# Optimization experiments

Hardware: AMD Instinct MI355X
Metric: run time of the kernel (lower is better)

## Reference

```python
import jax, jax.numpy as jnp
import numpy as np

B, L, H, V = 64, 2048, 256, 32000
BETA = 0.9
EPS_K = 1e-6   # delta-rule key-norm eps (matches torch 1e-06)
EPS_LN = 1e-5  # torch LayerNorm default eps


def setup_inputs() -> dict:
    key = jax.random.key(0)
    ks = jax.random.split(key, 8)
    s = lambda k, shape: (jax.random.normal(k, shape, jnp.float32) * 0.02)
    return {
        "seq": jax.random.randint(ks[0], (B, L), 0, V),
        "embed": s(ks[1], (V, H)),
        "W1": s(ks[2], (H, 2 * H)),
        "b1": jnp.zeros((2 * H,), jnp.float32),
        "W2": s(ks[3], (2 * H, H)),
        "b2": jnp.zeros((H,), jnp.float32),
        "gamma": jnp.ones((H,), jnp.float32),
        "beta_ln": jnp.zeros((H,), jnp.float32),
        "rp_W": s(ks[4], (H, H)),
        "rp_b": jnp.zeros((H,), jnp.float32),
        "out_W": s(ks[5], (H, V)),
        "out_b": jnp.zeros((V,), jnp.float32),
    }


def reference(seq, embed, W1, b1, W2, b2, gamma, beta_ln, rp_W, rp_b, out_W, out_b):
    # Encoder: embed -> FFN residual -> LayerNorm
    e = embed[seq]                                    # [B, L, H]
    ff = jnp.maximum(e @ W1 + b1, 0.0) @ W2 + b2      # [B, L, H]
    x = e + ff
    mu = jnp.mean(x, axis=-1, keepdims=True)
    var = jnp.mean((x - mu) ** 2, axis=-1, keepdims=True)
    h_all = (x - mu) / jnp.sqrt(var + EPS_LN) * gamma + beta_ln  # [B, L, H]

    # Momentum delta-rule fast-weight memory over first L-1 steps (k == v == h_t)
    ks_t = jnp.moveaxis(h_all[:, :-1, :], 1, 0)       # [L-1, B, H] time-major

    def step(M, k):
        vp = jnp.einsum('bij,bj->bi', M, k)            # predicted value
        d = k - vp / (jnp.sum(k * k, axis=-1, keepdims=True) + EPS_K)
        delta = d[:, :, None] * k[:, None, :]          # outer product [B, H, H]
        return BETA * M + (1.0 - BETA) * delta, None

    M0 = jnp.zeros((h_all.shape[0], H, H), h_all.dtype)
    M, _ = jax.lax.scan(step, M0, ks_t)

    # Readout with final token
    y = jnp.einsum('bij,bj->bi', M, h_all[:, -1, :])   # [B, H]
    return (y @ rp_W + rp_b) @ out_W + out_b           # [B, V]
```

## Files before the change

kernel.cpp:

```cpp
#include <hip/hip_runtime.h>


#define B_ 64
#define L_ 2048
#define H_ 256
#define V_ 32000

typedef unsigned short u16;
typedef __attribute__((ext_vector_type(8))) short bf16x8;
typedef __attribute__((ext_vector_type(16))) float f32x16;
typedef __attribute__((ext_vector_type(4))) float f32x4;

__device__ __forceinline__ float b2f(u16 u){ union{unsigned x; float f;} z; z.x = ((unsigned)u)<<16; return z.f; }
__device__ __forceinline__ u16 f2b(float f){ union{float f; unsigned x;} z; z.f = f; unsigned r = z.x + 0x7FFFu + ((z.x>>16)&1u); return (u16)(r>>16); }
__device__ __forceinline__ float san(float v){ return (v == v && v > -1e30f && v < 1e30f) ? v : 0.f; }

template<bool F32> __device__ __forceinline__ float ldw(const void* p, long i){
  if (F32) return ((const float*)p)[i];
  return b2f(((const u16*)p)[i]);
}
template<bool F32> __device__ __forceinline__ float4 ld4(const void* p, long i){
  if (F32) return *(const float4*)((const float*)p + i);
  ushort4 u = *(const ushort4*)((const u16*)p + i);
  return make_float4(b2f(u.x), b2f(u.y), b2f(u.z), b2f(u.w));
}

__device__ __forceinline__ int detect_f32(const void* embed){
  const u16* e = (const u16*)embed;
  unsigned v = e[2 * (threadIdx.x & 255)];
  int ex = (v >> 7) & 0xFF;
  int pl = (ex >= 0x66 && ex <= 0x7D) || ((v & 0x7FFFu) == 0u);
  int cnt = __syncthreads_count(pl);
  return cnt < 128;
}

__global__ __launch_bounds__(256) void sentinel_kernel(const void* embed, void* out, float val)
{
  int f32 = detect_f32(embed);
  long idx = (long)blockIdx.x * 256 + threadIdx.x;
  if (idx < (long)B_ * V_){
    if (f32) ((float*)out)[idx] = val;
    else     ((u16*)out)[idx]   = f2b(val);
  }
}

template<bool F32>
__device__ __forceinline__ void wprep_body(
    const void* __restrict__ W1, const void* __restrict__ W2,
    u16* __restrict__ w1f_hi, u16* __restrict__ w1f_lo,
    u16* __restrict__ w2f_hi, u16* __restrict__ w2f_lo)
{
  const int cid = blockIdx.x * 256 + threadIdx.x;
  const int lane = cid & 63;
  const int nl = lane & 31, kh = lane >> 5;
  if (cid < 16384){
    const int nt = cid >> 10, k16 = (cid >> 6) & 15;
    const int n = nt*32 + nl;
    const int k0 = k16*16 + kh*8;
    #pragma unroll
    for (int e = 0; e < 8; ++e){
      float v = ldw<F32>(W1, (long)(k0+e)*512 + n);
      unsigned bi = __float_as_uint(v);
      u16 hi = (u16)(bi >> 16);
      float hif = __uint_as_float(((unsigned)hi) << 16);
      w1f_hi[cid*8 + e] = hi;
      w1f_lo[cid*8 + e] = f2b(v - hif);
    }
  } else {
    const int c2 = cid - 16384;
    const int nt = c2 >> 11, k16 = (c2 >> 6) & 31;
    const int n = nt*32 + nl;
    const int k0 = k16*16 + kh*8;
    #pragma unroll
    for (int e = 0; e < 8; ++e){
      float v = ldw<F32>(W2, (long)(k0+e)*256 + n);
      unsigned bi = __float_as_uint(v);
      u16 hi = (u16)(bi >> 16);
      float hif = __uint_as_float(((unsigned)hi) << 16);
      w2f_hi[c2*8 + e] = hi;
      w2f_lo[c2*8 + e] = f2b(v - hif);
    }
  }
}

__global__ __launch_bounds__(256) void wprep_kernel(
    const void* __restrict__ embed,
    const void* __restrict__ W1, const void* __restrict__ W2,
    u16* __restrict__ wbuf)
{
  u16* w1h = wbuf;
  u16* w1l = wbuf + 131072;
  u16* w2h = wbuf + 262144;
  u16* w2l = wbuf + 393216;
  if (detect_f32(embed)) wprep_body<true >(W1, W2, w1h, w1l, w2h, w2l);
  else                   wprep_body<false>(W1, W2, w1h, w1l, w2h, w2l);
}

template<bool F32>
__device__ __forceinline__ void encm_body(
    u16* e_l, u16* t1_l, float* red, float* red2, float* stats,
    const int* __restrict__ seq, const void* __restrict__ embed,
    const u16* __restrict__ w1f_hi, const u16* __restrict__ w1f_lo,
    const u16* __restrict__ w2f_hi, const u16* __restrict__ w2f_lo,
    const void* __restrict__ b1, const void* __restrict__ b2,
    const void* __restrict__ gamma, const void* __restrict__ beta,
    u16* __restrict__ h)
{
  const int tid = threadIdx.x;
  const long tok0 = (long)blockIdx.x * 32;
  const int lane = tid & 63, wv = tid >> 6;
  const int col = lane & 31, hw = lane >> 5;

  {
    const int tr = tid >> 3, u0 = (tid & 7) * 4;
    int tk = seq[tok0 + tr];
    tk = (tk >= 0 && tk < V_) ? tk : 0;
    #pragma unroll
    for (int c = 0; c < 4; ++c){
      const int u = u0 + c;
      const int phys = u ^ (tr & 7);
      if (F32){
        const float4* sp = (const float4*)((const float*)embed + (long)tk*H_ + u*8);
        float4 v0 = sp[0], v1 = sp[1];
        ushort4 o0, o1;
        o0.x=f2b(v0.x); o0.y=f2b(v0.y); o0.z=f2b(v0.z); o0.w=f2b(v0.w);
        o1.x=f2b(v1.x); o1.y=f2b(v1.y); o1.z=f2b(v1.z); o1.w=f2b(v1.w);
        *(ushort4*)&e_l[tr*256 + phys*8]     = o0;
        *(ushort4*)&e_l[tr*256 + phys*8 + 4] = o1;
      } else {
        uint4 v = *(const uint4*)((const u16*)embed + (long)tk*H_ + u*8);
        *(uint4*)&e_l[tr*256 + phys*8] = v;
      }
    }
  }
  __syncthreads();

  {
    f32x16 acc[4];
    #pragma unroll
    for (int t = 0; t < 4; ++t)
      #pragma unroll
      for (int r = 0; r < 16; ++r) acc[t][r] = 0.f;

    #pragma unroll
    for (int k16 = 0; k16 < 16; ++k16){
      const int phys = (k16*2 + hw) ^ (col & 7);
      bf16x8 a = *(const bf16x8*)&e_l[col*256 + phys*8];
      #pragma unroll
      for (int t = 0; t < 4; ++t){
        const int off = (((wv*4 + t)*16 + k16)*64 + lane)*8;
        bf16x8 bh = *(const bf16x8*)&w1f_hi[off];
        bf16x8 bl = *(const bf16x8*)&w1f_lo[off];
        acc[t] = __builtin_amdgcn_mfma_f32_32x32x16_bf16(a, bh, acc[t], 0, 0, 0);
        acc[t] = __builtin_amdgcn_mfma_f32_32x32x16_bf16(a, bl, acc[t], 0, 0, 0);
      }
    }

    #pragma unroll
    for (int t = 0; t < 4; ++t){
      const int n = (wv*4 + t)*32 + col;
      const float bb = ldw<F32>(b1, n);
      const int u = n >> 3, nl = n & 7;
      #pragma unroll
      for (int r = 0; r < 16; ++r){
        const int m = (r&3) + 8*(r>>2) + 4*hw;
        float v = fmaxf(acc[t][r] + bb, 0.f);
        t1_l[m*512 + ((u ^ (m&7))<<3) + nl] = f2b(v);
      }
    }
  }
  __syncthreads();

  f32x16 acc2[2];
  #pragma unroll
  for (int t = 0; t < 2; ++t)
    #pragma unroll
    for (int r = 0; r < 16; ++r) acc2[t][r] = 0.f;

  #pragma unroll
  for (int k16 = 0; k16 < 32; ++k16){
    const int phys = (k16*2 + hw) ^ (col & 7);
    bf16x8 a = *(const bf16x8*)&t1_l[col*512 + phys*8];
    #pragma unroll
    for (int t = 0; t < 2; ++t){
      const int off = (((wv*2 + t)*32 + k16)*64 + lane)*8;
      bf16x8 bh = *(const bf16x8*)&w2f_hi[off];
      bf16x8 bl = *(const bf16x8*)&w2f_lo[off];
      acc2[t] = __builtin_amdgcn_mfma_f32_32x32x16_bf16(a, bh, acc2[t], 0, 0, 0);
      acc2[t] = __builtin_amdgcn_mfma_f32_32x32x16_bf16(a, bl, acc2[t], 0, 0, 0);
    }
  }
  __syncthreads();

  u16* xb = t1_l;
  #pragma unroll
  for (int t = 0; t < 2; ++t){
    const int n = (wv*2 + t)*32 + col;
    const float bb = ldw<F32>(b2, n);
    const int ue = n >> 3, nl = n & 7;
    #pragma unroll
    for (int r = 0; r < 16; ++r){
      const int m = (r&3) + 8*(r>>2) + 4*hw;
      float ev = b2f(e_l[m*256 + ((ue ^ (m&7))<<3) + nl]);
      float x = acc2[t][r] + bb + ev;
      xb[m*256 + n] = f2b(x);
    }
  }
  __syncthreads();

  {
    const int row = tid >> 3, seg = tid & 7;
    const u16* xr = &xb[row*256 + seg*32];
    float s = 0.f, q = 0.f;
    #pragma unroll
    for (int j = 0; j < 32; j += 4){
      ushort4 v4 = *(const ushort4*)&xr[j];
      float v0 = b2f(v4.x), v1 = b2f(v4.y), v2 = b2f(v4.z), v3 = b2f(v4.w);
      s += v0 + v1 + v2 + v3;
      q += v0*v0 + v1*v1 + v2*v2 + v3*v3;
    }
    red[row*8 + seg] = s;
    red2[row*8 + seg] = q;
  }
  __syncthreads();
  if (tid < 32){
    float s = 0.f, q = 0.f;
    #pragma unroll
    for (int j = 0; j < 8; ++j){ s += red[tid*8 + j]; q += red2[tid*8 + j]; }
    float mu = s * (1.f/256.f);
    float var = q * (1.f/256.f) - mu*mu;
    stats[tid] = mu;
    stats[32 + tid] = 1.f / sqrtf(fmaxf(var, 0.f) + 1e-5f);
  }
  __syncthreads();

  {
    const int row = tid >> 3, c0 = (tid & 7) * 32;
    const float mu = stats[row], rs = stats[32 + row];
    u16* hp = h + (tok0 + row)*H_ + c0;
    const u16* xr = &xb[row*256 + c0];
    #pragma unroll
    for (int j = 0; j < 32; j += 4){
      float4 g  = ld4<F32>(gamma, c0 + j);
      float4 be = ld4<F32>(beta,  c0 + j);
      ushort4 xv = *(const ushort4*)&xr[j];
      ushort4 o;
      o.x = f2b(san((b2f(xv.x) - mu)*rs*g.x + be.x));
      o.y = f2b(san((b2f(xv.y) - mu)*rs*g.y + be.y));
      o.z = f2b(san((b2f(xv.z) - mu)*rs*g.z + be.z));
      o.w = f2b(san((b2f(xv.w) - mu)*rs*g.w + be.w));
      *(ushort4*)&hp[j] = o;
    }
  }
}

__global__ __launch_bounds__(256) void encm_kernel(
    const int* __restrict__ seq, const void* __restrict__ embed,
    const u16* __restrict__ wbuf,
    const void* __restrict__ b1, const void* __restrict__ b2,
    const void* __restrict__ gamma, const void* __restrict__ beta,
    u16* __restrict__ h)
{
  __shared__ __align__(16) u16 e_l[32*256];
  __shared__ __align__(16) u16 t1_l[32*512];
  __shared__ float red[256];
  __shared__ float red2[256];
  __shared__ float stats[64];
  const u16* w1h = wbuf;
  const u16* w1l = wbuf + 131072;
  const u16* w2h = wbuf + 262144;
  const u16* w2l = wbuf + 393216;
  if (detect_f32(embed))
    encm_body<true >(e_l, t1_l, red, red2, stats, seq, embed, w1h, w1l, w2h, w2l, b1, b2, gamma, beta, h);
  else
    encm_body<false>(e_l, t1_l, red, red2, stats, seq, embed, w1h, w1l, w2h, w2l, b1, b2, gamma, beta, h);
}

template<bool F32>
__device__ __forceinline__ void enc_body(
    u16* sm,
    const int* __restrict__ seq, const void* __restrict__ embed,
    const void* __restrict__ W1, const void* __restrict__ b1,
    const void* __restrict__ W2, const void* __restrict__ b2,
    const void* __restrict__ gamma, const void* __restrict__ beta,
    u16* __restrict__ h)
{
  u16* eT  = sm;
  u16* t1T = sm + 8192;
  u16* xb  = sm + 24576;
  float* stats = (float*)sm;

  const int tid = threadIdx.x;
  const long tok0 = (long)blockIdx.x * 32;

  for (int idx = tid; idx < 8192; idx += 256){
    int r = idx >> 8, c = idx & 255;
    int tk = seq[tok0 + r];
    tk = (tk >= 0 && tk < V_) ? tk : 0;
    eT[c*32 + r] = f2b(ldw<F32>(embed, (long)tk*H_ + c));
  }
  __syncthreads();

  const int jg = tid & 31, rg = tid >> 5;
  const int r0 = rg * 4;

  for (int sl = 0; sl < 4; ++sl){
    const int j0 = sl*128 + jg*4;
    float acc[4][4] = {{0.f}};
    for (int c = 0; c < 256; ++c){
      ushort4 a4 = *(const ushort4*)&eT[c*32 + r0];
      float4 w = ld4<F32>(W1, (long)c*512 + j0);
      float a0=b2f(a4.x), a1=b2f(a4.y), a2=b2f(a4.z), a3=b2f(a4.w);
      acc[0][0]+=a0*w.x; acc[0][1]+=a0*w.y; acc[0][2]+=a0*w.z; acc[0][3]+=a0*w.w;
      acc[1][0]+=a1*w.x; acc[1][1]+=a1*w.y; acc[1][2]+=a1*w.z; acc[1][3]+=a1*w.w;
      acc[2][0]+=a2*w.x; acc[2][1]+=a2*w.y; acc[2][2]+=a2*w.z; acc[2][3]+=a2*w.w;
      acc[3][0]+=a3*w.x; acc[3][1]+=a3*w.y; acc[3][2]+=a3*w.z; acc[3][3]+=a3*w.w;
    }
    for (int jj = 0; jj < 4; ++jj){
      float bb = ldw<F32>(b1, j0+jj);
      ushort4 o;
      o.x = f2b(fmaxf(acc[0][jj]+bb, 0.f));
      o.y = f2b(fmaxf(acc[1][jj]+bb, 0.f));
      o.z = f2b(fmaxf(acc[2][jj]+bb, 0.f));
      o.w = f2b(fmaxf(acc[3][jj]+bb, 0.f));
      *(ushort4*)&t1T[(j0+jj)*32 + r0] = o;
    }
  }
  __syncthreads();

  for (int sl = 0; sl < 2; ++sl){
    const int co0 = sl*128 + jg*4;
    float acc[4][4] = {{0.f}};
    for (int c = 0; c < 512; ++c){
      ushort4 a4 = *(const ushort4*)&t1T[c*32 + r0];
      float4 w = ld4<F32>(W2, (long)c*256 + co0);
      float a0=b2f(a4.x), a1=b2f(a4.y), a2=b2f(a4.z), a3=b2f(a4.w);
      acc[0][0]+=a0*w.x; acc[0][1]+=a0*w.y; acc[0][2]+=a0*w.z; acc[0][3]+=a0*w.w;
      acc[1][0]+=a1*w.x; acc[1][1]+=a1*w.y; acc[1][2]+=a1*w.z; acc[1][3]+=a1*w.w;
      acc[2][0]+=a2*w.x; acc[2][1]+=a2*w.y; acc[2][2]+=a2*w.z; acc[2][3]+=a2*w.w;
      acc[3][0]+=a3*w.x; acc[3][1]+=a3*w.y; acc[3][2]+=a3*w.z; acc[3][3]+=a3*w.w;
    }
    float bb0 = ldw<F32>(b2, co0+0), bb1 = ldw<F32>(b2, co0+1);
    float bb2 = ldw<F32>(b2, co0+2), bb3 = ldw<F32>(b2, co0+3);
    for (int rr = 0; rr < 4; ++rr){
      float x0 = acc[rr][0] + bb0 + b2f(eT[(co0+0)*32 + r0+rr]);
      float x1 = acc[rr][1] + bb1 + b2f(eT[(co0+1)*32 + r0+rr]);
      float x2 = acc[rr][2] + bb2 + b2f(eT[(co0+2)*32 + r0+rr]);
      float x3 = acc[rr][3] + bb3 + b2f(eT[(co0+3)*32 + r0+rr]);
      ushort4 o; o.x=f2b(x0); o.y=f2b(x1); o.z=f2b(x2); o.w=f2b(x3);
      *(ushort4*)&xb[(r0+rr)*256 + co0] = o;
    }
  }
  __syncthreads();

  if (tid < 32){
    float s = 0.f, q = 0.f;
    for (int c = 0; c < 256; ++c){ float v = b2f(xb[tid*256 + c]); s += v; q += v*v; }
    float mu = s * (1.f/256.f);
    float var = q * (1.f/256.f) - mu*mu;
    stats[tid] = mu;
    stats[32 + tid] = 1.f / sqrtf(fmaxf(var, 0.f) + 1e-5f);
  }
  __syncthreads();
  for (int idx = tid; idx < 8192; idx += 256){
    int r = idx >> 8, c = idx & 255;
    float hv = (b2f(xb[idx]) - stats[r]) * stats[32+r] * ldw<F32>(gamma, c) + ldw<F32>(beta, c);
    h[(tok0 + r)*H_ + c] = f2b(san(hv));
  }
}

__global__ __launch_bounds__(256) void enc_kernel(
    const int* __restrict__ seq, const void* __restrict__ embed,
    const void* __restrict__ W1, const void* __restrict__ b1,
    const void* __restrict__ W2, const void* __restrict__ b2,
    const void* __restrict__ gamma, const void* __restrict__ beta,
    u16* __restrict__ h)
{
  __shared__ __align__(16) u16 sm[32768];
  if (detect_f32(embed)) enc_body<true >(sm, seq, embed, W1, b1, W2, b2, gamma, beta, h);
  else                   enc_body<false>(sm, seq, embed, W1, b1, W2, b2, gamma, beta, h);
}

__global__ __launch_bounds__(64) void winv_kernel(
    const u16* __restrict__ h, u16* __restrict__ w2g, float* __restrict__ scg)
{
  __shared__ __align__(16) u16 k_l[32*256];
  __shared__ float g_l[32*33];
  __shared__ float w_l[32*33];
  __shared__ float bp[33];

  const int tid = threadIdx.x;
  const int cb = blockIdx.x;
  const int b = cb >> 6, ch = cb & 63;
  const int col = tid & 31, hw = tid >> 5;
  const int C = (ch == 63) ? 31 : 32;

  if (tid < 33) bp[tid] = powf(0.9f, (float)tid);

  {
    const int t = tid >> 1, u0 = (tid & 1) * 16;
    const u16* src = h + ((long)b*L_ + ch*32 + t)*H_ + u0*8;
    #pragma unroll
    for (int c = 0; c < 16; ++c){
      uint4 v = make_uint4(0u,0u,0u,0u);
      if (t < C) v = *(const uint4*)(src + c*8);
      int phys = (u0 + c) ^ (t & 7);
      *(uint4*)&k_l[t*256 + phys*8] = v;
    }
  }
  __syncthreads();

  {
    f32x16 acc; for (int r = 0; r < 16; ++r) acc[r] = 0.f;
    #pragma unroll
    for (int s = 0; s < 16; ++s){
      int phys = (s*2 + hw) ^ (col & 7);
      bf16x8 a = *(const bf16x8*)&k_l[col*256 + phys*8];
      acc = __builtin_amdgcn_mfma_f32_32x32x16_bf16(a, a, acc, 0, 0, 0);
    }
    #pragma unroll
    for (int r = 0; r < 16; ++r){
      int row = (r&3) + 8*(r>>2) + 4*hw;
      g_l[row*33 + col] = acc[r];
    }
  }
  __syncthreads();

  if (tid < 32){
    const int c = tid;
    for (int t = 0; t < 32; ++t){
      float acc = (t == c) ? 1.f : 0.f;
      if (t > c){
        float f = 0.1f / (g_l[t*33 + t] + 1e-6f);
        for (int s = c; s < t; ++s)
          acc -= f * bp[t-1-s] * g_l[t*33 + s] * w_l[s*33 + c];
      }
      w_l[t*33 + c] = acc;
    }
    scg[(long)cb*32 + c] = bp[c] / (g_l[c*33 + c] + 1e-6f);
  }
  __syncthreads();

  for (int idx = tid; idx < 1024; idx += 64){
    int t = idx >> 5, s = idx & 31;
    float v = 0.f;
    if (t < C && s <= t) v = 0.1f * bp[C-1-t] * w_l[t*33 + s];
    w2g[(long)cb*1024 + idx] = f2b(v);
  }
}

__global__ __launch_bounds__(512, 4) void scan_big(
    const u16* __restrict__ h, const u16* __restrict__ w2g,
    const float* __restrict__ scg, float* __restrict__ y)
{
  __shared__ __align__(16) u16   k_l[2][32*256];
  __shared__ __align__(16) u16   M_hi[32*256];
  __shared__ __align__(16) u16   M_lo[32*256];
  __shared__ float u_p[32*33];
  __shared__ __align__(16) u16   w2_l[32*32];
  __shared__ __align__(16) u16   dwT[32*32];
  __shared__ float sc_l[32];

  const int tid = threadIdx.x;
  const int b = blockIdx.x & 63, ib = blockIdx.x >> 6;
  const int lane = tid & 63, wv = tid >> 6;
  const int col = lane & 31, hw = lane >> 5;

  const u16*  hb  = h   + (long)b * L_ * H_;
  const u16*  w2b = w2g + (long)b * 64 * 1024;
  const float* scb = scg + (long)b * 64 * 32;

  const float b31 = powf(0.9f, 31.0f);
  const float b32 = b31 * 0.9f;

  for (int idx = tid; idx < 1024; idx += 512){
    ((uint4*)M_hi)[idx] = make_uint4(0u,0u,0u,0u);
    ((uint4*)M_lo)[idx] = make_uint4(0u,0u,0u,0u);
  }
  if (tid < 256){
    const int st = tid >> 3, su0 = (tid & 7) * 4;
    const u16* src = hb + (long)st * H_ + su0 * 8;
    #pragma unroll
    for (int c = 0; c < 4; ++c){
      uint4 v = *(const uint4*)(src + c*8);
      *(uint4*)&k_l[0][st*256 + ((su0+c)^(st&7))*8] = v;
    }
    *(uint2*)&w2_l[tid*4] = *(const uint2*)(w2b + tid*4);
    if (tid < 32) sc_l[tid] = scb[tid];
  }
  __syncthreads();

  for (int ch = 0; ch < 64; ++ch){
    const int cur = ch & 1, nxt = cur ^ 1;
    const float bC = (ch == 63) ? b31 : b32;

    uint2 pw = make_uint2(0u,0u); float psc = 0.f;

    if (wv < 4){
      const int th = wv & 1, ih = wv >> 1;
      const int li = lane & 15, kg = lane >> 4;
      const int t = th*16 + li;
      const int i = ih*16 + li;
      const int tx = t & 7, ix = i & 7;
      const u16* kr  = &k_l[cur][t*256];
      const u16* mhr = &M_hi[i*256];
      const u16* mlr = &M_lo[i*256];
      f32x4 a0, a1;
      #pragma unroll
      for (int r = 0; r < 4; ++r){ a0[r] = 0.f; a1[r] = 0.f; }
      #pragma unroll
      for (int ks = 0; ks < 8; ++ks){
        const int u = ks*4 + kg;
        bf16x8 a  = *(const bf16x8*)&kr[(u ^ tx)*8];
        bf16x8 bh = *(const bf16x8*)&mhr[(u ^ ix)*8];
        bf16x8 bl = *(const bf16x8*)&mlr[(u ^ ix)*8];
        if (ks & 1){
          a1 = __builtin_amdgcn_mfma_f32_16x16x32_bf16(a, bh, a1, 0, 0, 0);
          a1 = __builtin_amdgcn_mfma_f32_16x16x32_bf16(a, bl, a1, 0, 0, 0);
        } else {
          a0 = __builtin_amdgcn_mfma_f32_16x16x32_bf16(a, bh, a0, 0, 0, 0);
          a0 = __builtin_amdgcn_mfma_f32_16x16x32_bf16(a, bl, a0, 0, 0, 0);
        }
      }
      #pragma unroll
      for (int r = 0; r < 4; ++r)
        u_p[(th*16 + kg*4 + r)*33 + i] = a0[r] + a1[r];
    } else {
      const int s = tid - 256;
      const int st = s >> 3, su0 = (s & 7) * 4;
      const int chn = (ch < 63) ? ch + 1 : 63;
      const long tg = (long)chn*32 + st;
      const u16* src = hb + tg * H_ + su0 * 8;
      uint4 pf[4];
      #pragma unroll
      for (int c = 0; c < 4; ++c) pf[c] = *(const uint4*)(src + c*8);
      if (tg >= 2047){
        #pragma unroll
        for (int c = 0; c < 4; ++c) pf[c] = make_uint4(0u,0u,0u,0u);
      }
      pw = *(const uint2*)(w2b + chn*1024 + s*4);
      psc = (s < 32) ? scb[chn*32 + s] : 0.f;
      #pragma unroll
      for (int c = 0; c < 4; ++c)
        *(uint4*)&k_l[nxt][st*256 + ((su0+c)^(st&7))*8] = pf[c];
    }
    __syncthreads();

    if (wv == 0){
      const int jg = ib*32 + col;
      const int ju = jg >> 3, jo = jg & 7;
      bf16x8 bh0, bl0, bh1, bl1;
      #pragma unroll
      for (int c = 0; c < 8; ++c){
        const int t = hw*8 + c;
        float u = u_p[t*33 + col];
        float kti = b2f(k_l[cur][t*256 + ((ju ^ (t&7))<<3) + jo]);
        float r = kti - sc_l[t]*u;
        unsigned bi = __float_as_uint(r);
        bh0[c] = (short)(bi >> 16);
        bl0[c] = (short)f2b(r - __uint_as_float(bi & 0xFFFF0000u));
        const int t2 = t + 16;
        float u2 = u_p[t2*33 + col];
        float kti2 = b2f(k_l[cur][t2*256 + ((ju ^ (t2&7))<<3) + jo]);
        float r2 = kti2 - sc_l[t2]*u2;
        unsigned bi2 = __float_as_uint(r2);
        bh1[c] = (short)(bi2 >> 16);
        bl1[c] = (short)f2b(r2 - __uint_as_float(bi2 & 0xFFFF0000u));
      }
      f32x16 d0, d1;
      #pragma unroll
      for (int r = 0; r < 16; ++r){ d0[r] = 0.f; d1[r] = 0.f; }
      {
        bf16x8 aw0 = *(const bf16x8*)&w2_l[col*32 + hw*8];
        bf16x8 aw1 = *(const bf16x8*)&w2_l[col*32 + 16 + hw*8];
        d0 = __builtin_amdgcn_mfma_f32_32x32x16_bf16(aw0, bh0, d0, 0, 0, 0);
        d0 = __builtin_amdgcn_mfma_f32_32x32x16_bf16(aw0, bl0, d0, 0, 0, 0);
        d1 = __builtin_amdgcn_mfma_f32_32x32x16_bf16(aw1, bh1, d1, 0, 0, 0);
        d1 = __builtin_amdgcn_mfma_f32_32x32x16_bf16(aw1, bl1, d1, 0, 0, 0);
      }
      #pragma unroll
      for (int g = 0; g < 4; ++g){
        ushort4 o;
        o.x = f2b(d0[4*g+0] + d1[4*g+0]);
        o.y = f2b(d0[4*g+1] + d1[4*g+1]);
        o.z = f2b(d0[4*g+2] + d1[4*g+2]);
        o.w = f2b(d0[4*g+3] + d1[4*g+3]);
        *(ushort4*)&dwT[col*32 + 8*g + 4*hw] = o;
      }
    }
    __syncthreads();

    {
      bf16x8 bD0 = *(const bf16x8*)&dwT[col*32 + hw*8];
      bf16x8 bD1 = *(const bf16x8*)&dwT[col*32 + 16 + hw*8];
      const int j = wv*32 + col;
      const int ju = j >> 3, jo = j & 7;
      bf16x8 aK0, aK1;
      #pragma unroll
      for (int c = 0; c < 8; ++c){
        const int t = hw*8 + c;
        aK0[c] = (short)k_l[cur][t*256 + ((ju ^ (t&7))<<3) + jo];
        const int t2 = t + 16;
        aK1[c] = (short)k_l[cur][t2*256 + ((ju ^ (t2&7))<<3) + jo];
      }
      f32x16 macc;
      #pragma unroll
      for (int r = 0; r < 16; ++r) macc[r] = 0.f;
      macc = __builtin_amdgcn_mfma_f32_32x32x16_bf16(aK0, bD0, macc, 0, 0, 0);
      macc = __builtin_amdgcn_mfma_f32_32x32x16_bf16(aK1, bD1, macc, 0, 0, 0);
      #pragma unroll
      for (int g = 0; g < 4; ++g){
        const int u = wv*4 + g;
        const int addr = col*256 + ((u ^ (col&7))<<3) + 4*hw;
        ushort4 mh = *(ushort4*)&M_hi[addr];
        ushort4 ml = *(ushort4*)&M_lo[addr];
        ushort4 nh, nl;
        #pragma unroll
        for (int e = 0; e < 4; ++e){
          float f = b2f((&mh.x)[e]) + b2f((&ml.x)[e]);
          float nv = bC*f + macc[4*g + e];
          unsigned bi = __float_as_uint(nv);
          u16 hi = (u16)(bi >> 16);
          (&nh.x)[e] = hi;
          (&nl.x)[e] = f2b(nv - __uint_as_float(((unsigned)hi) << 16));
        }
        *(ushort4*)&M_hi[addr] = nh;
        *(ushort4*)&M_lo[addr] = nl;
      }
    }
    if (wv >= 4){
      const int s = tid - 256;
      *(uint2*)&w2_l[s*4] = pw;
      if (s < 32) sc_l[s] = psc;
    }
    __syncthreads();
  }

  float* q_l = u_p;
  float* par = u_p + 256;
  if (tid < 256) q_l[tid] = b2f(hb[(long)(L_-1)*H_ + tid]);
  __syncthreads();
  {
    const int i = tid & 31, pt = tid >> 5;
    float s = 0.f;
    #pragma unroll
    for (int jj = 0; jj < 16; ++jj){
      const int j = pt*16 + jj;
      const int addr = i*256 + (((j>>3) ^ (i&7))<<3) + (j&7);
      s += (b2f(M_hi[addr]) + b2f(M_lo[addr])) * q_l[j];
    }
    par[pt*32 + i] = s;
  }
  __syncthreads();
  if (tid < 32){
    float s = 0.f;
    #pragma unroll
    for (int pt = 0; pt < 16; ++pt) s += par[pt*32 + tid];
    y[b*H_ + ib*32 + tid] = san(s);
  }
}

__global__ __launch_bounds__(128) void scan_fallback(
    const u16* __restrict__ h, float* __restrict__ y)
{
  __shared__ __align__(16) float M_l[32*257];
  __shared__ __align__(16) u16  k_l[32*256];
  __shared__ float d_l[32*33];
  __shared__ float g_l[32*33];
  __shared__ float bp[33];

  const int tid = threadIdx.x;
  const int b = blockIdx.x & 63, ib = blockIdx.x >> 6;
  const int lane = tid & 63, wv = tid >> 6;
  const int col = lane & 31, hw = lane >> 5;

  for (int idx = tid; idx < 32*257; idx += 128) M_l[idx] = 0.f;
  if (tid < 33) bp[tid] = powf(0.9f, (float)tid);
  const u16* hb = h + (long)b * L_ * H_;
  __syncthreads();

  for (int ch = 0; ch < 64; ++ch){
    const int t0 = ch*32;
    const int C = (2047 - t0 < 32) ? (2047 - t0) : 32;

    {
      const int t = tid >> 2, j0 = (tid & 3) * 64;
      const uint4* gp = (const uint4*)(hb + (long)(t0 + t)*H_ + j0);
      #pragma unroll
      for (int c = 0; c < 8; ++c){
        uint4 v = (t < C) ? gp[c] : make_uint4(0u,0u,0u,0u);
        int phys = ((j0 >> 3) + c) ^ (t & 7);
        *(uint4*)&k_l[t*256 + phys*8] = v;
      }
    }
    __syncthreads();

    if (wv == 1){
      f32x16 acc; for (int r=0;r<16;++r) acc[r]=0.f;
      #pragma unroll
      for (int s = 0; s < 16; ++s){
        int phys = (s*2 + hw) ^ (col & 7);
        bf16x8 a = *(const bf16x8*)&k_l[col*256 + phys*8];
        acc = __builtin_amdgcn_mfma_f32_32x32x16_bf16(a, a, acc, 0, 0, 0);
      }
      #pragma unroll
      for (int r = 0; r < 16; ++r){
        int row = (r&3) + 8*(r>>2) + 4*hw;
        g_l[row*33 + col] = acc[r];
      }
    } else {
      f32x16 acc; for (int r=0;r<16;++r) acc[r]=0.f;
      for (int s = 0; s < 16; ++s){
        int phys = (s*2 + hw) ^ (col & 7);
        bf16x8 a = *(const bf16x8*)&k_l[col*256 + phys*8];
        bf16x8 bh, bl;
        const float* mp = &M_l[col*257 + s*16 + hw*8];
        #pragma unroll
        for (int c = 0; c < 8; ++c){
          float f = mp[c];
          unsigned bi = __float_as_uint(f);
          bh[c] = (short)(bi >> 16);
          float hif = __uint_as_float(bi & 0xFFFF0000u);
          bl[c] = (short)f2b(f - hif);
        }
        acc = __builtin_amdgcn_mfma_f32_32x32x16_bf16(a, bh, acc, 0, 0, 0);
        acc = __builtin_amdgcn_mfma_f32_32x32x16_bf16(a, bl, acc, 0, 0, 0);
      }
      #pragma unroll
      for (int r = 0; r < 16; ++r){
        int row = (r&3) + 8*(r>>2) + 4*hw;
        d_l[row*33 + col] = acc[r];
      }
    }
    __syncthreads();

    #pragma unroll
    for (int p = 0; p < 8; ++p){
      int idx = p*128 + tid;
      int t = idx >> 5, i = idx & 31;
      float u = d_l[t*33 + i];
      int jg = ib*32 + i;
      float kti = b2f(k_l[t*256 + (((jg>>3) ^ (t&7))<<3) + (jg&7)]);
      float inv = 1.f / (g_l[t*33 + t] + 1e-6f);
      d_l[t*33 + i] = kti - bp[t] * u * inv;
    }
    __syncthreads();

    if (tid < 32){
      const int c = tid;
      for (int t = 1; t < C; ++t){
        float f = 0.1f / (g_l[t*33 + t] + 1e-6f);
        float acc = d_l[t*33 + c];
        for (int s = 0; s < t; ++s)
          acc -= f * bp[t-1-s] * g_l[t*33 + s] * d_l[s*33 + c];
        d_l[t*33 + c] = acc;
      }
    }
    __syncthreads();

    {
      const float bC = bp[C];
      bf16x8 bfr[2];
      #pragma unroll
      for (int h2 = 0; h2 < 2; ++h2){
        #pragma unroll
        for (int c = 0; c < 8; ++c){
          int t = h2*16 + hw*8 + c;
          int ci = C-1-t;
          float w = (ci >= 0) ? 0.1f * bp[ci] : 0.f;
          bfr[h2][c] = (short)f2b(d_l[t*33 + col] * w);
        }
      }
      for (int jt = wv*4; jt < wv*4 + 4; ++jt){
        f32x16 acc; for (int r=0;r<16;++r) acc[r]=0.f;
        #pragma unroll
        for (int h2 = 0; h2 < 2; ++h2){
          bf16x8 a;
          int j = jt*32 + col;
          #pragma unroll
          for (int c = 0; c < 8; ++c){
            int t = h2*16 + hw*8 + c;
            a[c] = (short)k_l[t*256 + (((j>>3) ^ (t&7))<<3) + (j&7)];
          }
          acc = __builtin_amdgcn_mfma_f32_32x32x16_bf16(a, bfr[h2], acc, 0, 0, 0);
        }
        #pragma unroll
        for (int r = 0; r < 16; ++r){
          int jrow = jt*32 + (r&3) + 8*(r>>2) + 4*hw;
          int addr = col*257 + jrow;
          M_l[addr] = bC * M_l[addr] + acc[r];
        }
      }
    }
    __syncthreads();
  }

  float* q_l = g_l;
  for (int p = tid; p < 256; p += 128) q_l[p] = b2f(hb[(long)(L_-1)*H_ + p]);
  __syncthreads();
  {
    int i = tid & 31, pt = tid >> 5;
    float s = 0.f;
    const float* mp = &M_l[i*257 + pt*64];
    const float* qp = &q_l[pt*64];
    for (int jj = 0; jj < 64; ++jj) s += mp[jj] * qp[jj];
    d_l[pt*33 + i] = s;
  }
  __syncthreads();
  if (tid < 32){
    float s = d_l[tid] + d_l[33 + tid] + d_l[66 + tid] + d_l[99 + tid];
    y[b*H_ + ib*32 + tid] = san(s);
  }
}

template<bool F32>
__device__ __forceinline__ void r1_body(
    float* yl, const float* __restrict__ y, const void* __restrict__ rpW,
    const void* __restrict__ rpb, float* __restrict__ zT)
{
  const int b = blockIdx.x, tid = threadIdx.x;
  yl[tid] = san(y[b*H_ + tid]);
  __syncthreads();
  float acc = ldw<F32>(rpb, tid);
  for (int j = 0; j < 256; ++j) acc += yl[j] * ldw<F32>(rpW, (long)j*H_ + tid);
  zT[tid*B_ + b] = san(acc);
}

__global__ __launch_bounds__(256) void r1_kernel(
    const void* __restrict__ embed, const float* __restrict__ y,
    const void* __restrict__ rpW, const void* __restrict__ rpb,
    float* __restrict__ zT)
{
  __shared__ float yl[256];
  if (detect_f32(embed)) r1_body<true >(yl, y, rpW, rpb, zT);
  else                   r1_body<false>(yl, y, rpW, rpb, zT);
}

template<bool F32>
__device__ __forceinline__ void r2_body(
    float* zl, const float* __restrict__ zT, const void* __restrict__ outW,
    const void* __restrict__ outb, void* __restrict__ out)
{
  const int tid = threadIdx.x;
  const int v = blockIdx.x*256 + tid;
  for (int idx = tid; idx < 16384; idx += 256) zl[idx] = zT[idx];
  __syncthreads();

  float ob = ldw<F32>(outb, v);
  float acc[64];
  #pragma unroll
  for (int bb = 0; bb < 64; ++bb) acc[bb] = ob;

  for (int i = 0; i < 256; ++i){
    float w = ldw<F32>(outW, (long)i*V_ + v);
    const float4* zp = (const float4*)&zl[i*64];
    #pragma unroll
    for (int q = 0; q < 16; ++q){
      float4 z4 = zp[q];
      acc[q*4+0] += w*z4.x; acc[q*4+1] += w*z4.y;
      acc[q*4+2] += w*z4.z; acc[q*4+3] += w*z4.w;
    }
  }
  if (F32){
    for (int bb = 0; bb < 64; ++bb) ((float*)out)[(long)bb*V_ + v] = san(acc[bb]);
  } else {
    for (int bb = 0; bb < 64; ++bb) ((u16*)out)[(long)bb*V_ + v] = f2b(san(acc[bb]));
  }
}

__global__ __launch_bounds__(256) void r2_kernel(
    const void* __restrict__ embed, const float* __restrict__ zT,
    const void* __restrict__ outW, const void* __restrict__ outb,
    void* __restrict__ out)
{
  __shared__ float zl[16384];
  if (detect_f32(embed)) r2_body<true >(zl, zT, outW, outb, out);
  else                   r2_body<false>(zl, zT, outW, outb, out);
}

extern "C" void kernel_launch(void* const* d_in, const int* in_sizes, int n_in,
                              void* d_out, int out_size, void* d_ws, size_t ws_size,
                              hipStream_t stream) {
  bool sizes_ok = (n_in == 12) && in_sizes
      && in_sizes[0] == B_*L_ && in_sizes[1] == V_*H_ && in_sizes[2] == H_*2*H_
      && in_sizes[3] == 2*H_  && in_sizes[4] == 2*H_*H_ && in_sizes[5] == H_
      && in_sizes[6] == H_    && in_sizes[7] == H_    && in_sizes[8] == H_*H_
      && in_sizes[9] == H_    && in_sizes[10] == H_*V_ && in_sizes[11] == V_;
  if (!sizes_ok){
    sentinel_kernel<<<(B_*V_ + 255)/256, 256, 0, stream>>>(d_in ? d_in[1] : d_out, d_out, 2000.0f);
    return;
  }
  if (ws_size < 67108864ull){
    sentinel_kernel<<<(B_*V_ + 255)/256, 256, 0, stream>>>(d_in[1], d_out, 1000.0f);
    return;
  }

  const int* seq   = (const int*)d_in[0];
  const void* embed= d_in[1];
  const void* W1   = d_in[2];
  const void* b1   = d_in[3];
  const void* W2   = d_in[4];
  const void* b2   = d_in[5];
  const void* gamma= d_in[6];
  const void* beta = d_in[7];
  const void* rpW  = d_in[8];
  const void* rpb  = d_in[9];
  const void* outW = d_in[10];
  const void* outb = d_in[11];

  u16*   h  = (u16*)d_ws;
  float* zT = (float*)d_ws;
  float* y  = (float*)d_out;

  const size_t need = 67108864ull + 8388608ull + 524288ull;
  if (ws_size >= need){
    u16*   wbuf = (u16*)  ((char*)d_ws + 67108864);
    u16*   w2g  = (u16*)  ((char*)d_ws + 67108864);
    float* scg  = (float*)((char*)d_ws + 67108864 + 8388608);
    wprep_kernel<<< 128, 256, 0, stream>>>(embed, W1, W2, wbuf);
    encm_kernel <<<4096, 256, 0, stream>>>(seq, embed, wbuf, b1, b2, gamma, beta, h);
    winv_kernel <<<4096,  64, 0, stream>>>(h, w2g, scg);
    scan_big    <<< 512, 512, 0, stream>>>(h, w2g, scg, y);
  } else {
    enc_kernel<<<4096, 256, 0, stream>>>(seq, embed, W1, b1, W2, b2, gamma, beta, h);
    scan_fallback<<<512, 128, 0, stream>>>(h, y);
  }

  r1_kernel<<< 64, 256, 0, stream>>>(embed, y, rpW, rpb, zT);
  r2_kernel<<<125, 256, 0, stream>>>(embed, zT, outW, outb, d_out);
}
```

Baseline: 748.5 us.

## Widen scan_big row tile to 64 and keep fp32 M state in registers

Each scan block now owns 64 rows of the fast-weight matrix instead of 32, which halves the grid to 256 blocks and halves redundant per-block reloads of k chunks and chunk weights. All 8 waves now share the u-projection (split into hi and lo parts), the dW computation and the M update, with prefetch handled by every thread rather than a dedicated wave group. The M state is kept in fp32 registers across chunks and written to LDS only as a hi/lo bf16 split for the next chunk's MFMA, which removes the per-step LDS read-modify-write. The trade-off is fewer blocks (less parallelism across CUs), larger LDS and register use, and a launch bound lowered to 2 blocks per CU.

```diff
diff --git a/kernel.cpp b/kernel.cpp
--- a/kernel.cpp
+++ b/kernel.cpp
@@ -449,22 +449,23 @@
   }
 }
 
-__global__ __launch_bounds__(512, 4) void scan_big(
+__global__ __launch_bounds__(512, 2) void scan_big(
     const u16* __restrict__ h, const u16* __restrict__ w2g,
     const float* __restrict__ scg, float* __restrict__ y)
 {
   __shared__ __align__(16) u16   k_l[2][32*256];
-  __shared__ __align__(16) u16   M_hi[32*256];
-  __shared__ __align__(16) u16   M_lo[32*256];
-  __shared__ float u_p[32*33];
-  __shared__ __align__(16) u16   w2_l[32*32];
-  __shared__ __align__(16) u16   dwT[32*32];
+  __shared__ __align__(16) u16   M_hi[64*256];
+  __shared__ __align__(16) u16   M_lo[64*256];
+  __shared__ float u_p[2][32*66];
+  __shared__ __align__(16) u16   w2_l[32*40];
+  __shared__ __align__(16) u16   dwT[64*40];
   __shared__ float sc_l[32];
 
   const int tid = threadIdx.x;
   const int b = blockIdx.x & 63, ib = blockIdx.x >> 6;
   const int lane = tid & 63, wv = tid >> 6;
   const int col = lane & 31, hw = lane >> 5;
+  const int li = lane & 15, kg = lane >> 4;
 
   const u16*  hb  = h   + (long)b * L_ * H_;
   const u16*  w2b = w2g + (long)b * 64 * 1024;
@@ -473,19 +474,25 @@
   const float b31 = powf(0.9f, 31.0f);
   const float b32 = b31 * 0.9f;
 
-  for (int idx = tid; idx < 1024; idx += 512){
+  f32x16 Mr0, Mr1;
+  #pragma unroll
+  for (int r = 0; r < 16; ++r){ Mr0[r] = 0.f; Mr1[r] = 0.f; }
+
+  for (int idx = tid; idx < 2048; idx += 512){
     ((uint4*)M_hi)[idx] = make_uint4(0u,0u,0u,0u);
     ((uint4*)M_lo)[idx] = make_uint4(0u,0u,0u,0u);
   }
-  if (tid < 256){
-    const int st = tid >> 3, su0 = (tid & 7) * 4;
-    const u16* src = hb + (long)st * H_ + su0 * 8;
-    #pragma unroll
-    for (int c = 0; c < 4; ++c){
-      uint4 v = *(const uint4*)(src + c*8);
-      *(uint4*)&k_l[0][st*256 + ((su0+c)^(st&7))*8] = v;
-    }
-    *(uint2*)&w2_l[tid*4] = *(const uint2*)(w2b + tid*4);
+  {
+    const int st = tid >> 4;
+    const int sp = (tid & 15) * 2;
+    const u16* src = hb + (long)st * H_ + sp * 8;
+    uint4 v0 = *(const uint4*)(src);
+    uint4 v1 = *(const uint4*)(src + 8);
+    *(uint4*)&k_l[0][st*256 + (((sp  ) ^ (st&7))<<3)] = v0;
+    *(uint4*)&k_l[0][st*256 + (((sp+1) ^ (st&7))<<3)] = v1;
+    unsigned wval = *(const unsigned*)(w2b + tid*2);
+    int t = (tid*2) >> 5, s = (tid*2) & 31;
+    *(unsigned*)&w2_l[t*40 + s] = wval;
     if (tid < 32) sc_l[tid] = scb[tid];
   }
   __syncthreads();
@@ -494,169 +501,167 @@
     const int cur = ch & 1, nxt = cur ^ 1;
     const float bC = (ch == 63) ? b31 : b32;
 
-    uint2 pw = make_uint2(0u,0u); float psc = 0.f;
-
-    if (wv < 4){
-      const int th = wv & 1, ih = wv >> 1;
-      const int li = lane & 15, kg = lane >> 4;
-      const int t = th*16 + li;
-      const int i = ih*16 + li;
-      const int tx = t & 7, ix = i & 7;
-      const u16* kr  = &k_l[cur][t*256];
-      const u16* mhr = &M_hi[i*256];
-      const u16* mlr = &M_lo[i*256];
+    uint4 pf0, pf1; unsigned pw; float psc = 0.f;
+    {
+      const int chn = (ch < 63) ? ch + 1 : 63;
+      const int st = tid >> 4, sp = (tid & 15) * 2;
+      const long tg = (long)chn*32 + st;
+      const u16* src = hb + tg * H_ + sp * 8;
+      pf0 = *(const uint4*)(src);
+      pf1 = *(const uint4*)(src + 8);
+      if (tg >= 2047){ pf0 = make_uint4(0u,0u,0u,0u); pf1 = make_uint4(0u,0u,0u,0u); }
+      pw = *(const unsigned*)(w2b + chn*1024 + tid*2);
+      if (tid < 32) psc = scb[chn*32 + tid];
+    }
+
+    {
+      const int th = wv & 1, ihh = (wv >> 1) & 1, part = wv >> 2;
+      const u16* Mp = part ? M_lo : M_hi;
+      const int t  = th*16 + li;
+      const int i0 = ihh*32 + li;
+      const int i1 = i0 + 16;
+      const int tx = t & 7, ix = li & 7;
       f32x4 a0, a1;
       #pragma unroll
       for (int r = 0; r < 4; ++r){ a0[r] = 0.f; a1[r] = 0.f; }
       #pragma unroll
       for (int ks = 0; ks < 8; ++ks){
         const int u = ks*4 + kg;
-        bf16x8 a  = *(const bf16x8*)&kr[(u ^ tx)*8];
-        bf16x8 bh = *(const bf16x8*)&mhr[(u ^ ix)*8];
-        bf16x8 bl = *(const bf16x8*)&mlr[(u ^ ix)*8];
-        if (ks & 1){
-          a1 = __builtin_amdgcn_mfma_f32_16x16x32_bf16(a, bh, a1, 0, 0, 0);
-          a1 = __builtin_amdgcn_mfma_f32_16x16x32_bf16(a, bl, a1, 0, 0, 0);
-        } else {
-          a0 = __builtin_amdgcn_mfma_f32_16x16x32_bf16(a, bh, a0, 0, 0, 0);
-          a0 = __builtin_amdgcn_mfma_f32_16x16x32_bf16(a, bl, a0, 0, 0, 0);
-        }
-      }
-      #pragma unroll
-      for (int r = 0; r < 4; ++r)
-        u_p[(th*16 + kg*4 + r)*33 + i] = a0[r] + a1[r];
-    } else {
-      const int s = tid - 256;
-      const int st = s >> 3, su0 = (s & 7) * 4;
-      const int chn = (ch < 63) ? ch + 1 : 63;
-      const long tg = (long)chn*32 + st;
-      const u16* src = hb + tg * H_ + su0 * 8;
-      uint4 pf[4];
-      #pragma unroll
-      for (int c = 0; c < 4; ++c) pf[c] = *(const uint4*)(src + c*8);
-      if (tg >= 2047){
-        #pragma unroll
-        for (int c = 0; c < 4; ++c) pf[c] = make_uint4(0u,0u,0u,0u);
-      }
-      pw = *(const uint2*)(w2b + chn*1024 + s*4);
-      psc = (s < 32) ? scb[chn*32 + s] : 0.f;
-      #pragma unroll
-      for (int c = 0; c < 4; ++c)
-        *(uint4*)&k_l[nxt][st*256 + ((su0+c)^(st&7))*8] = pf[c];
+        bf16x8 a  = *(const bf16x8*)&k_l[cur][t*256 + ((u ^ tx)<<3)];
+        bf16x8 b0 = *(const bf16x8*)&Mp[i0*256 + ((u ^ ix)<<3)];
+        bf16x8 b1 = *(const bf16x8*)&Mp[i1*256 + ((u ^ ix)<<3)];
+        a0 = __builtin_amdgcn_mfma_f32_16x16x32_bf16(a, b0, a0, 0, 0, 0);
+        a1 = __builtin_amdgcn_mfma_f32_16x16x32_bf16(a, b1, a1, 0, 0, 0);
+      }
+      #pragma unroll
+      for (int r = 0; r < 4; ++r){
+        const int trow = th*16 + kg*4 + r;
+        u_p[part][trow*66 + i0] = a0[r];
+        u_p[part][trow*66 + i1] = a1[r];
+      }
     }
     __syncthreads();
 
-    if (wv == 0){
-      const int jg = ib*32 + col;
-      const int ju = jg >> 3, jo = jg & 7;
-      bf16x8 bh0, bl0, bh1, bl1;
+    {
+      const int t_h = wv & 1, i_q = wv >> 1;
+      const int i  = i_q*16 + li;
+      const int ig = ib*64 + i;
+      const int ju = ig >> 3, jo = ig & 7;
+      bf16x8 bh, bl;
+      #pragma unroll
+      for (int e = 0; e < 8; ++e){
+        const int s = kg*8 + e;
+        float u = u_p[0][s*66 + i] + u_p[1][s*66 + i];
+        float kti = b2f(k_l[cur][s*256 + ((ju ^ (s&7))<<3) + jo]);
+        float r = kti - sc_l[s]*u;
+        unsigned bi = __float_as_uint(r);
+        bh[e] = (short)(bi >> 16);
+        bl[e] = (short)f2b(r - __uint_as_float(bi & 0xFFFF0000u));
+      }
+      bf16x8 aw = *(const bf16x8*)&w2_l[(t_h*16 + li)*40 + kg*8];
+      f32x4 dacc;
+      #pragma unroll
+      for (int r = 0; r < 4; ++r) dacc[r] = 0.f;
+      dacc = __builtin_amdgcn_mfma_f32_16x16x32_bf16(aw, bh, dacc, 0, 0, 0);
+      dacc = __builtin_amdgcn_mfma_f32_16x16x32_bf16(aw, bl, dacc, 0, 0, 0);
+      ushort4 o;
+      o.x = f2b(dacc[0]); o.y = f2b(dacc[1]);
+      o.z = f2b(dacc[2]); o.w = f2b(dacc[3]);
+      *(ushort4*)&dwT[i*40 + t_h*16 + kg*4] = o;
+    }
+    __syncthreads();
+
+    {
+      const int j  = wv*32 + col;
+      const int ju = j >> 3, jo = j & 7;
+      bf16x8 aK0, aK1;
       #pragma unroll
       for (int c = 0; c < 8; ++c){
         const int t = hw*8 + c;
-        float u = u_p[t*33 + col];
-        float kti = b2f(k_l[cur][t*256 + ((ju ^ (t&7))<<3) + jo]);
-        float r = kti - sc_l[t]*u;
-        unsigned bi = __float_as_uint(r);
-        bh0[c] = (short)(bi >> 16);
-        bl0[c] = (short)f2b(r - __uint_as_float(bi & 0xFFFF0000u));
-        const int t2 = t + 16;
-        float u2 = u_p[t2*33 + col];
-        float kti2 = b2f(k_l[cur][t2*256 + ((ju ^ (t2&7))<<3) + jo]);
-        float r2 = kti2 - sc_l[t2]*u2;
-        unsigned bi2 = __float_as_uint(r2);
-        bh1[c] = (short)(bi2 >> 16);
-        bl1[c] = (short)f2b(r2 - __uint_as_float(bi2 & 0xFFFF0000u));
-      }
-      f32x16 d0, d1;
-      #pragma unroll
-      for (int r = 0; r < 16; ++r){ d0[r] = 0.f; d1[r] = 0.f; }
+        const int base = t*256 + ((ju ^ (t&7))<<3) + jo;
+        aK0[c] = (short)k_l[cur][base];
+        aK1[c] = (short)k_l[cur][base + 4096];
+      }
       {
-        bf16x8 aw0 = *(const bf16x8*)&w2_l[col*32 + hw*8];
-        bf16x8 aw1 = *(const bf16x8*)&w2_l[col*32 + 16 + hw*8];
-        d0 = __builtin_amdgcn_mfma_f32_32x32x16_bf16(aw0, bh0, d0, 0, 0, 0);
-        d0 = __builtin_amdgcn_mfma_f32_32x32x16_bf16(aw0, bl0, d0, 0, 0, 0);
-        d1 = __builtin_amdgcn_mfma_f32_32x32x16_bf16(aw1, bh1, d1, 0, 0, 0);
-        d1 = __builtin_amdgcn_mfma_f32_32x32x16_bf16(aw1, bl1, d1, 0, 0, 0);
-      }
-      #pragma unroll
-      for (int g = 0; g < 4; ++g){
-        ushort4 o;
-        o.x = f2b(d0[4*g+0] + d1[4*g+0]);
-        o.y = f2b(d0[4*g+1] + d1[4*g+1]);
-        o.z = f2b(d0[4*g+2] + d1[4*g+2]);
-        o.w = f2b(d0[4*g+3] + d1[4*g+3]);
-        *(ushort4*)&dwT[col*32 + 8*g + 4*hw] = o;
-      }
-    }
-    __syncthreads();
-
-    {
-      bf16x8 bD0 = *(const bf16x8*)&dwT[col*32 + hw*8];
-      bf16x8 bD1 = *(const bf16x8*)&dwT[col*32 + 16 + hw*8];
-      const int j = wv*32 + col;
-      const int ju = j >> 3, jo = j & 7;
-      bf16x8 aK0, aK1;
-      #pragma unroll
-      for (int c = 0; c < 8; ++c){
-        const int t = hw*8 + c;
-        aK0[c] = (short)k_l[cur][t*256 + ((ju ^ (t&7))<<3) + jo];
-        const int t2 = t + 16;
-        aK1[c] = (short)k_l[cur][t2*256 + ((ju ^ (t2&7))<<3) + jo];
-      }
-      f32x16 macc;
-      #pragma unroll
-      for (int r = 0; r < 16; ++r) macc[r] = 0.f;
-      macc = __builtin_amdgcn_mfma_f32_32x32x16_bf16(aK0, bD0, macc, 0, 0, 0);
-      macc = __builtin_amdgcn_mfma_f32_32x32x16_bf16(aK1, bD1, macc, 0, 0, 0);
+        bf16x8 bD0 = *(const bf16x8*)&dwT[col*40 + hw*8];
+        bf16x8 bD1 = *(const bf16x8*)&dwT[col*40 + 16 + hw*8];
+        f32x16 macc;
+        #pragma unroll
+        for (int r = 0; r < 16; ++r) macc[r] = 0.f;
+        macc = __builtin_amdgcn_mfma_f32_32x32x16_bf16(aK0, bD0, macc, 0, 0, 0);
+        macc = __builtin_amdgcn_mfma_f32_32x32x16_bf16(aK1, bD1, macc, 0, 0, 0);
+        #pragma unroll
+        for (int r = 0; r < 16; ++r) Mr0[r] = bC*Mr0[r] + macc[r];
+      }
+      {
+        bf16x8 bD0 = *(const bf16x8*)&dwT[(col + 32)*40 + hw*8];
+        bf16x8 bD1 = *(const bf16x8*)&dwT[(col + 32)*40 + 16 + hw*8];
+        f32x16 macc;
+        #pragma unroll
+        for (int r = 0; r < 16; ++r) macc[r] = 0.f;
+        macc = __builtin_amdgcn_mfma_f32_32x32x16_bf16(aK0, bD0, macc, 0, 0, 0);
+        macc = __builtin_amdgcn_mfma_f32_32x32x16_bf16(aK1, bD1, macc, 0, 0, 0);
+        #pragma unroll
+        for (int r = 0; r < 16; ++r) Mr1[r] = bC*Mr1[r] + macc[r];
+      }
+      const int ix0 = col & 7;
       #pragma unroll
       for (int g = 0; g < 4; ++g){
         const int u = wv*4 + g;
-        const int addr = col*256 + ((u ^ (col&7))<<3) + 4*hw;
-        ushort4 mh = *(ushort4*)&M_hi[addr];
-        ushort4 ml = *(ushort4*)&M_lo[addr];
-        ushort4 nh, nl;
+        ushort4 nh0, nl0, nh1, nl1;
         #pragma unroll
         for (int e = 0; e < 4; ++e){
-          float f = b2f((&mh.x)[e]) + b2f((&ml.x)[e]);
-          float nv = bC*f + macc[4*g + e];
-          unsigned bi = __float_as_uint(nv);
-          u16 hi = (u16)(bi >> 16);
-          (&nh.x)[e] = hi;
-          (&nl.x)[e] = f2b(nv - __uint_as_float(((unsigned)hi) << 16));
+          float v0 = Mr0[4*g + e];
+          unsigned b0 = __float_as_uint(v0);
+          u16 h0 = (u16)(b0 >> 16);
+          (&nh0.x)[e] = h0;
+          (&nl0.x)[e] = f2b(v0 - __uint_as_float(((unsigned)h0) << 16));
+          float v1 = Mr1[4*g + e];
+          unsigned b1 = __float_as_uint(v1);
+          u16 h1 = (u16)(b1 >> 16);
+          (&nh1.x)[e] = h1;
+          (&nl1.x)[e] = f2b(v1 - __uint_as_float(((unsigned)h1) << 16));
         }
-        *(ushort4*)&M_hi[addr] = nh;
-        *(ushort4*)&M_lo[addr] = nl;
-      }
-    }
-    if (wv >= 4){
-      const int s = tid - 256;
-      *(uint2*)&w2_l[s*4] = pw;
-      if (s < 32) sc_l[s] = psc;
+        const int a0 = col*256 + ((u ^ ix0)<<3) + 4*hw;
+        const int a1 = (col+32)*256 + ((u ^ ix0)<<3) + 4*hw;
+        *(ushort4*)&M_hi[a0] = nh0;
+        *(ushort4*)&M_lo[a0] = nl0;
+        *(ushort4*)&M_hi[a1] = nh1;
+        *(ushort4*)&M_lo[a1] = nl1;
+      }
+      const int st = tid >> 4, sp = (tid & 15) * 2;
+      *(uint4*)&k_l[nxt][st*256 + (((sp  ) ^ (st&7))<<3)] = pf0;
+      *(uint4*)&k_l[nxt][st*256 + (((sp+1) ^ (st&7))<<3)] = pf1;
+      {
+        int t = (tid*2) >> 5, s = (tid*2) & 31;
+        *(unsigned*)&w2_l[t*40 + s] = pw;
+      }
+      if (tid < 32) sc_l[tid] = psc;
     }
     __syncthreads();
   }
 
-  float* q_l = u_p;
-  float* par = u_p + 256;
+  float* q_l = (float*)u_p;
+  float* par = ((float*)u_p) + 256;
   if (tid < 256) q_l[tid] = b2f(hb[(long)(L_-1)*H_ + tid]);
   __syncthreads();
   {
-    const int i = tid & 31, pt = tid >> 5;
+    float q_r[16];
+    #pragma unroll
+    for (int r = 0; r < 16; ++r)
+      q_r[r] = q_l[wv*32 + (r&3) + 8*(r>>2) + 4*hw];
+    float s0 = 0.f, s1 = 0.f;
+    #pragma unroll
+    for (int r = 0; r < 16; ++r){ s0 += Mr0[r]*q_r[r]; s1 += Mr1[r]*q_r[r]; }
+    par[(wv*2 + hw)*64 + col]      = s0;
+    par[(wv*2 + hw)*64 + col + 32] = s1;
+  }
+  __syncthreads();
+  if (tid < 64){
     float s = 0.f;
     #pragma unroll
-    for (int jj = 0; jj < 16; ++jj){
-      const int j = pt*16 + jj;
-      const int addr = i*256 + (((j>>3) ^ (i&7))<<3) + (j&7);
-      s += (b2f(M_hi[addr]) + b2f(M_lo[addr])) * q_l[j];
-    }
-    par[pt*32 + i] = s;
-  }
-  __syncthreads();
-  if (tid < 32){
-    float s = 0.f;
-    #pragma unroll
-    for (int pt = 0; pt < 16; ++pt) s += par[pt*32 + tid];
-    y[b*H_ + ib*32 + tid] = san(s);
+    for (int p = 0; p < 16; ++p) s += par[p*64 + tid];
+    y[b*H_ + ib*64 + tid] = san(s);
   }
 }
 
@@ -920,7 +925,7 @@
     wprep_kernel<<< 128, 256, 0, stream>>>(embed, W1, W2, wbuf);
     encm_kernel <<<4096, 256, 0, stream>>>(seq, embed, wbuf, b1, b2, gamma, beta, h);
     winv_kernel <<<4096,  64, 0, stream>>>(h, w2g, scg);
-    scan_big    <<< 512, 512, 0, stream>>>(h, w2g, scg, y);
+    scan_big    <<< 256, 512, 0, stream>>>(h, w2g, scg, y);
   } else {
     enc_kernel<<<4096, 256, 0, stream>>>(seq, embed, W1, b1, W2, b2, gamma, beta, h);
     scan_fallback<<<512, 128, 0, stream>>>(h, y);
```

After: 686.4 us, median of 2. 8.3% less time.
